# Kernel optimization log

Measured on AMD Instinct MI355X. Metric: run time of the kernel, lower is better.

## Reference

```python
import math
import jax, jax.numpy as jnp
import numpy as np

B, N, E, H = 1, 4096, 256, 8
D = E // H  # head dim = 32


def setup_inputs() -> dict:
    key = jax.random.key(0)
    ks = jax.random.split(key, 10)
    s = 1.0 / math.sqrt(E)
    return {
        "x": jax.random.normal(ks[0], (B, N, E), dtype=jnp.float32),
        "adjacency": jax.random.randint(ks[1], (B, N, N), 0, 2, dtype=jnp.int32),
        "Wq": jax.random.normal(ks[2], (E, E), dtype=jnp.float32) * s,
        "bq": jnp.zeros((E,), dtype=jnp.float32),
        "Wk": jax.random.normal(ks[3], (E, E), dtype=jnp.float32) * s,
        "bk": jnp.zeros((E,), dtype=jnp.float32),
        "Wv": jax.random.normal(ks[4], (E, E), dtype=jnp.float32) * s,
        "bv": jnp.zeros((E,), dtype=jnp.float32),
        "Wo": jax.random.normal(ks[5], (E, E), dtype=jnp.float32) * s,
        "bo": jnp.zeros((E,), dtype=jnp.float32),
    }


def reference(x, adjacency, Wq, bq, Wk, bk, Wv, bv, Wo, bo):
    b, n, e = x.shape
    # projections (torch Linear: x @ W.T + b), split into heads -> [B,H,N,D]
    def heads(y):
        return y.reshape(b, n, H, D).transpose(0, 2, 1, 3)
    q = heads(x @ Wq.T + bq)
    k = heads(x @ Wk.T + bk)
    v = heads(x @ Wv.T + bv)
    scores = jnp.einsum("bhnd,bhmd->bhnm", q, k) / math.sqrt(D)
    mask = (adjacency[:, None, :, :] == 0)  # [B,1,N,N]
    scores = jnp.where(mask, -jnp.inf, scores)
    w = jax.nn.softmax(scores, axis=-1)
    out = jnp.einsum("bhnm,bhmd->bhnd", w, v)
    out = out.transpose(0, 2, 1, 3).reshape(b, n, e)
    return out @ Wo.T + bo
```

## Files before the change

kernel.cpp:

```cpp
#include <hip/hip_runtime.h>
#include <math.h>


#define NTOK 4096
#define EDIM 256
#define HEADS 8
#define HD 32
#define NSPLIT 2
#define QSCALE 0.17677669529663687f
#define LOG2E 1.4426950408889634f
#define CINIT (-11.541560327111707f)

typedef __attribute__((ext_vector_type(8))) short bf16x8;
typedef __attribute__((ext_vector_type(4))) float f32x4;
typedef __attribute__((ext_vector_type(4))) unsigned long long u64x4;

typedef __attribute__((address_space(3))) unsigned char lds_u8;
typedef const __attribute__((address_space(1))) unsigned char gl_u8;

static __device__ inline short f2bf(float f) {
    unsigned u = __float_as_uint(f);
    u = (u + 0x7FFFu + ((u >> 16) & 1u)) >> 16;
    return (short)u;
}
static __device__ inline unsigned packtrunc(float a, float b) {
    return __builtin_amdgcn_perm(__float_as_uint(b), __float_as_uint(a),
                                 0x07060302u);
}
static __device__ inline float sel_mask(float v, unsigned long long m) {
    float r;
    asm("v_cndmask_b32 %0, 0, %1, %2" : "=v"(r) : "v"(v), "s"(m));
    return r;
}

__global__ __launch_bounds__(256) void prep(
    const int* __restrict__ adj, unsigned long long* __restrict__ maskT,
    const float* __restrict__ x,  const float* __restrict__ Wq,
    const float* __restrict__ Wk, const float* __restrict__ Wv,
    const float* __restrict__ Wo,
    short* __restrict__ xb,  short* __restrict__ wqb,
    short* __restrict__ wkb, short* __restrict__ wvb,
    short* __restrict__ wob)
{
    const int bid = blockIdx.x;
    if (bid < 2048) {
        const int wb = bid * 4 + (threadIdx.x >> 6);
        const int l = threadIdx.x & 63;
        const int lrow = l & 15;
        const int lc4 = ((l >> 4) & 3) * 4;
#pragma unroll
        for (int i = 0; i < 8; ++i) {
            const int w = wb + i * 8192;
            const int qb = w >> 8;
            const int kt = (w >> 2) & 63;
            const int b = w & 3;
            const int row = qb * 16 + lrow;
            const int col = kt * 64 + b * 16 + lc4;
            const int4 av = *(const int4*)&adj[row * NTOK + col];
            const unsigned long long m0 = __ballot(av.x != 0);
            const unsigned long long m1 = __ballot(av.y != 0);
            const unsigned long long m2 = __ballot(av.z != 0);
            const unsigned long long m3 = __ballot(av.w != 0);
            if (l == 0) {
                unsigned long long* dst = &maskT[(size_t)w * 4];
                dst[0] = m0; dst[1] = m1; dst[2] = m2; dst[3] = m3;
            }
        }
    } else {
        const int gid = (bid - 2048) * 256 + threadIdx.x;
        const int e = gid * 4;
        const float* src; short* dst; int off;
        if (e < NTOK * EDIM) { src = x; dst = xb; off = e; }
        else {
            const int r = e - NTOK * EDIM;
            const int wsel = r >> 16;
            off = r & 65535;
            src = (wsel == 0) ? Wq : (wsel == 1) ? Wk : (wsel == 2) ? Wv : Wo;
            dst = (wsel == 0) ? wqb : (wsel == 1) ? wkb : (wsel == 2) ? wvb : wob;
        }
        float4 v = *(const float4*)&src[off];
        uint2 t;
        t.x = (unsigned short)f2bf(v.x) | ((unsigned)(unsigned short)f2bf(v.y) << 16);
        t.y = (unsigned short)f2bf(v.z) | ((unsigned)(unsigned short)f2bf(v.w) << 16);
        *(uint2*)&dst[off] = t;
    }
}

__global__ __launch_bounds__(256) void qkv_mfma(
    const short* __restrict__ xb,
    const short* __restrict__ Wqb, const short* __restrict__ Wkb,
    const short* __restrict__ Wvb,
    const float* __restrict__ bq, const float* __restrict__ bk,
    const float* __restrict__ bv,
    short* __restrict__ qo, short* __restrict__ ko, short* __restrict__ vto)
{
    const int tid = threadIdx.x;
    const int wv = tid >> 6, lane = tid & 63;
    const int grp = lane >> 4, lcol = lane & 15;
    const int wsel = blockIdx.y >> 2;
    const int n0 = (blockIdx.y & 3) << 6;
    const int m0 = blockIdx.x * 64 + wv * 16;
    const short* __restrict__ W = (wsel == 0) ? Wqb : (wsel == 1) ? Wkb : Wvb;
    const float* __restrict__ bias = (wsel == 0) ? bq : (wsel == 1) ? bk : bv;

    bf16x8 af[8];
#pragma unroll
    for (int k = 0; k < 8; ++k)
        af[k] = *(const bf16x8*)&xb[(m0 + lcol) * 256 + k * 32 + grp * 8];

    f32x4 acc[4] = {};
#pragma unroll
    for (int k = 0; k < 8; ++k) {
#pragma unroll
        for (int t = 0; t < 4; ++t) {
            const bf16x8 bt =
                *(const bf16x8*)&W[(n0 + t * 16 + lcol) * 256 + k * 32 + grp * 8];
            acc[t] = __builtin_amdgcn_mfma_f32_16x16x32_bf16(af[k], bt, acc[t], 0, 0, 0);
        }
    }
#pragma unroll
    for (int t = 0; t < 4; ++t) {
        const int feat = n0 + t * 16 + lcol;
        const float bval = bias[feat];
        const int h = feat >> 5, d = feat & 31;
        if (wsel == 2) {
            uint2 o;
            o.x = (unsigned short)f2bf(acc[t][0] + bval) |
                  ((unsigned)(unsigned short)f2bf(acc[t][1] + bval) << 16);
            o.y = (unsigned short)f2bf(acc[t][2] + bval) |
                  ((unsigned)(unsigned short)f2bf(acc[t][3] + bval) << 16);
            *(uint2*)&vto[h * (HD * NTOK) + d * NTOK + m0 + grp * 4] = o;
        } else {
            short* __restrict__ out = (wsel == 0) ? qo : ko;
            const float sc = (wsel == 0) ? (QSCALE * LOG2E) : 1.0f;
#pragma unroll
            for (int j = 0; j < 4; ++j)
                out[h * (NTOK * HD) + (m0 + grp * 4 + j) * HD + d] =
                    f2bf((acc[t][j] + bval) * sc);
        }
    }
}

__global__ __launch_bounds__(256) void attn_mfma(
    const short* __restrict__ qg, const short* __restrict__ kg,
    const short* __restrict__ vtg, const unsigned long long* __restrict__ maskT,
    float* __restrict__ o_part, float* __restrict__ l_part)
{
    const int h = blockIdx.y;
    const int split = blockIdx.z;
    const int q0 = blockIdx.x << 6;
    const short* __restrict__ Q  = qg  + h * (NTOK * HD);
    const short* __restrict__ K  = kg  + h * (NTOK * HD);
    const short* __restrict__ Vt = vtg + h * (HD * NTOK);

    __shared__ short Ks[3][64][32];
    __shared__ short Vs[3][32][64];
    __shared__ short P_lds[4][16][76];

    const int tid = threadIdx.x;
    const int wv = tid >> 6;
    const int lane = tid & 63;
    const int grp = lane >> 4;
    const int lcol = lane & 15;
    const int q0w = q0 + wv * 16;
    const int wvu = __builtin_amdgcn_readfirstlane(wv);

    const int k_row = tid >> 2, k_oct = tid & 3;
    const int v_row = tid >> 3;
    const int v_oct = (tid & 7) ^ (v_row & 7);
    const short* __restrict__ kbase = &K[k_row * HD + k_oct * 8];
    const short* __restrict__ vbase = &Vt[v_row * NTOK + v_oct * 8];

    const bf16x8 qfrag = *(const bf16x8*)&Q[(q0w + lcol) * HD + grp * 8];

    const int qb = __builtin_amdgcn_readfirstlane(blockIdx.x * 4 + wv);
    const unsigned long long* __restrict__ mbase = maskT + (size_t)qb * 1024;

    f32x4 ot[2] = {};
    f32x4 lacc = {};
    const f32x4 cinit = {CINIT, CINIT, CINIT, CINIT};
    bf16x8 ones;
#pragma unroll
    for (int i = 0; i < 8; ++i) ones[i] = (short)0x3F80;

    const int tps = 64 / (int)gridDim.z;
    const int kt_begin = split * tps;
    const int kt_end = kt_begin + tps;

#define STAGE(BUF, KT)                                                       \
    {                                                                        \
        const int k0s = (KT) << 6;                                           \
        __builtin_amdgcn_global_load_lds(                                    \
            (gl_u8*)(kbase + k0s * HD),                                      \
            (lds_u8*)((unsigned char*)&Ks[BUF][0][0] + (wvu << 10)),         \
            16, 0, 0);                                                       \
        __builtin_amdgcn_global_load_lds(                                    \
            (gl_u8*)(vbase + k0s),                                           \
            (lds_u8*)((unsigned char*)&Vs[BUF][0][0] + (wvu << 10)),         \
            16, 0, 0);                                                       \
    }

    STAGE(0, kt_begin)
    if (kt_begin + 1 < kt_end) STAGE(1, kt_begin + 1)

    int cur = 0;
    for (int kt = kt_begin; kt < kt_end; ++kt) {
        if (kt + 1 < kt_end)
            asm volatile("s_waitcnt vmcnt(2)" ::: "memory");
        else
            asm volatile("s_waitcnt vmcnt(0)" ::: "memory");
        __builtin_amdgcn_s_barrier();
        __builtin_amdgcn_sched_barrier(0);

        const u64x4* mp = (const u64x4*)(mbase + kt * 16);
        const u64x4 wa = mp[0], wb = mp[1], wc = mp[2], wd = mp[3];

        const int nxt = (cur == 0) ? 2 : cur - 1;
        if (kt + 2 < kt_end) STAGE(nxt, kt + 2)

        bf16x8 kf[4], vf[4];
#pragma unroll
        for (int b = 0; b < 4; ++b)
            kf[b] = *(const bf16x8*)&Ks[cur][b * 16 + lcol][grp * 8];
#pragma unroll
        for (int c = 0; c < 2; ++c) {
            vf[c * 2 + 0] =
                *(const bf16x8*)&Vs[cur][c * 16 + lcol][(grp ^ (lcol & 7)) * 8];
            vf[c * 2 + 1] =
                *(const bf16x8*)&Vs[cur][c * 16 + lcol][((4 + grp) ^ (lcol & 7)) * 8];
        }

        f32x4 s[4];
        __builtin_amdgcn_s_setprio(1);
#pragma unroll
        for (int b = 0; b < 4; ++b)
            s[b] = __builtin_amdgcn_mfma_f32_16x16x32_bf16(
                kf[b], qfrag, cinit, 0, 0, 0);
        __builtin_amdgcn_s_setprio(0);

#pragma unroll
        for (int b = 0; b < 4; ++b) {
            const u64x4 wj = (b == 0) ? wa : (b == 1) ? wb : (b == 2) ? wc : wd;
            const float p0 = sel_mask(__builtin_amdgcn_exp2f(s[b][0]), wj[0]);
            const float p1 = sel_mask(__builtin_amdgcn_exp2f(s[b][1]), wj[1]);
            const float p2 = sel_mask(__builtin_amdgcn_exp2f(s[b][2]), wj[2]);
            const float p3 = sel_mask(__builtin_amdgcn_exp2f(s[b][3]), wj[3]);
            uint2 t;
            t.x = packtrunc(p0, p1);
            t.y = packtrunc(p2, p3);
            *(uint2*)&P_lds[wv][lcol][b * 16 + grp * 4] = t;
        }

        const uint2 pl0 = *(const uint2*)&P_lds[wv][lcol][grp * 8];
        const uint2 pl1 = *(const uint2*)&P_lds[wv][lcol][grp * 8 + 4];
        const uint2 pl2 = *(const uint2*)&P_lds[wv][lcol][32 + grp * 8];
        const uint2 pl3 = *(const uint2*)&P_lds[wv][lcol][32 + grp * 8 + 4];
        struct { uint2 a, b; } u0 = {pl0, pl1}, u1 = {pl2, pl3};
        const bf16x8 pf0 = __builtin_bit_cast(bf16x8, u0);
        const bf16x8 pf1 = __builtin_bit_cast(bf16x8, u1);

        __builtin_amdgcn_s_setprio(1);
#pragma unroll
        for (int c = 0; c < 2; ++c) {
            ot[c] = __builtin_amdgcn_mfma_f32_16x16x32_bf16(vf[c * 2 + 0], pf0, ot[c], 0, 0, 0);
            ot[c] = __builtin_amdgcn_mfma_f32_16x16x32_bf16(vf[c * 2 + 1], pf1, ot[c], 0, 0, 0);
        }
        lacc = __builtin_amdgcn_mfma_f32_16x16x32_bf16(ones, pf0, lacc, 0, 0, 0);
        lacc = __builtin_amdgcn_mfma_f32_16x16x32_bf16(ones, pf1, lacc, 0, 0, 0);
        __builtin_amdgcn_s_setprio(0);

        cur = (cur == 2) ? 0 : cur + 1;
    }
#undef STAGE

    float* __restrict__ ob = o_part + split * (NTOK * EDIM);
#pragma unroll
    for (int c = 0; c < 2; ++c) {
        float4 st;
        st.x = ot[c][0]; st.y = ot[c][1]; st.z = ot[c][2]; st.w = ot[c][3];
        *(float4*)&ob[(q0w + lcol) * EDIM + h * HD + c * 16 + grp * 4] = st;
    }
    if (grp == 0)
        l_part[split * (NTOK * HEADS) + (q0w + lcol) * HEADS + h] = lacc[0];
}

template <int NS>
__global__ __launch_bounds__(256) void out_mfma(
    const float* __restrict__ o_part, const float* __restrict__ l_part,
    const short* __restrict__ Wob, const float* __restrict__ bo,
    float* __restrict__ Y)
{
    const int tid = threadIdx.x;
    const int wv = tid >> 6, lane = tid & 63;
    const int grp = lane >> 4, lcol = lane & 15;
    const int n0 = blockIdx.y << 6;
    const int m0 = blockIdx.x * 64 + wv * 16;
    const int r = m0 + lcol;

    bf16x8 af[8];
#pragma unroll
    for (int k = 0; k < 8; ++k) {
        float4 s0 = {0.f, 0.f, 0.f, 0.f}, s1 = {0.f, 0.f, 0.f, 0.f};
        float lv = 0.f;
#pragma unroll
        for (int s = 0; s < NS; ++s) {
            const float* op = &o_part[s * (NTOK * EDIM) + r * EDIM + k * 32 + grp * 8];
            const float4 t0 = *(const float4*)op;
            const float4 t1 = *(const float4*)(op + 4);
            s0.x += t0.x; s0.y += t0.y; s0.z += t0.z; s0.w += t0.w;
            s1.x += t1.x; s1.y += t1.y; s1.z += t1.z; s1.w += t1.w;
            lv += l_part[s * (NTOK * HEADS) + r * HEADS + k];
        }
        const float inv = 1.0f / lv;
        bf16x8 t;
        t[0] = f2bf(s0.x * inv); t[1] = f2bf(s0.y * inv);
        t[2] = f2bf(s0.z * inv); t[3] = f2bf(s0.w * inv);
        t[4] = f2bf(s1.x * inv); t[5] = f2bf(s1.y * inv);
        t[6] = f2bf(s1.z * inv); t[7] = f2bf(s1.w * inv);
        af[k] = t;
    }

    f32x4 acc[4] = {};
#pragma unroll
    for (int k = 0; k < 8; ++k) {
#pragma unroll
        for (int t = 0; t < 4; ++t) {
            const bf16x8 bt =
                *(const bf16x8*)&Wob[(n0 + t * 16 + lcol) * 256 + k * 32 + grp * 8];
            acc[t] = __builtin_amdgcn_mfma_f32_16x16x32_bf16(af[k], bt, acc[t], 0, 0, 0);
        }
    }
#pragma unroll
    for (int t = 0; t < 4; ++t) {
        const float bval = bo[n0 + t * 16 + lcol];
#pragma unroll
        for (int j = 0; j < 4; ++j)
            Y[(m0 + grp * 4 + j) * EDIM + n0 + t * 16 + lcol] = acc[t][j] + bval;
    }
}

extern "C" void kernel_launch(void* const* d_in, const int* in_sizes, int n_in,
                              void* d_out, int out_size, void* d_ws, size_t ws_size,
                              hipStream_t stream) {
    (void)in_sizes; (void)n_in; (void)out_size; (void)ws_size;
    const float* x  = (const float*)d_in[0];
    const int*  adj = (const int*)d_in[1];
    const float* Wq = (const float*)d_in[2];
    const float* bq = (const float*)d_in[3];
    const float* Wk = (const float*)d_in[4];
    const float* bk = (const float*)d_in[5];
    const float* Wv = (const float*)d_in[6];
    const float* bv = (const float*)d_in[7];
    const float* Wo = (const float*)d_in[8];
    const float* bo = (const float*)d_in[9];

    char* ws = (char*)d_ws;
    short* x_bf  = (short*)(ws);
    short* q_ws  = (short*)(ws + (2u << 20));
    short* k_ws  = (short*)(ws + (4u << 20));
    short* vt_ws = (short*)(ws + (6u << 20));
    unsigned long long* maskT =
        (unsigned long long*)(ws + (8u << 20));
    short* Wq_bf = (short*)(ws + (10u << 20));
    short* Wk_bf = Wq_bf + (EDIM * EDIM);
    short* Wv_bf = Wk_bf + (EDIM * EDIM);
    short* Wo_bf = Wv_bf + (EDIM * EDIM);
    float* l_part = (float*)(ws + (11u << 20));
    float* o_part = (float*)(ws + (12u << 20));

    prep<<<dim3(2048 + 1280), 256, 0, stream>>>(
        adj, maskT, x, Wq, Wk, Wv, Wo, x_bf, Wq_bf, Wk_bf, Wv_bf, Wo_bf);
    qkv_mfma<<<dim3(64, 12), 256, 0, stream>>>(x_bf, Wq_bf, Wk_bf, Wv_bf,
                                               bq, bk, bv, q_ws, k_ws, vt_ws);
    attn_mfma<<<dim3(64, HEADS, NSPLIT), 256, 0, stream>>>(
        q_ws, k_ws, vt_ws, maskT, o_part, l_part);
    out_mfma<NSPLIT><<<dim3(64, 4), 256, 0, stream>>>(o_part, l_part, Wo_bf, bo,
                                                      (float*)d_out);
}
```

Before: 175.4 us.

## Process two KV tiles per barrier with a four-buffer pipeline

The attention main loop now handles two 64-key tiles per iteration, using four K/V LDS buffers and double-buffered P scratch. This halves the number of workgroup barriers and waitcnt points and lets two tiles' prefetch be issued together. In exchange it waits with vmcnt(0) every pair, which can expose load latency, and it raises LDS use, which may lower occupancy. It also assumes an even tile count per split.

```diff
diff --git a/kernel.cpp b/kernel.cpp
--- a/kernel.cpp
+++ b/kernel.cpp
@@ -153,9 +153,9 @@
     const short* __restrict__ K  = kg  + h * (NTOK * HD);
     const short* __restrict__ Vt = vtg + h * (HD * NTOK);
 
-    __shared__ short Ks[3][64][32];
-    __shared__ short Vs[3][32][64];
-    __shared__ short P_lds[4][16][76];
+    __shared__ short Ks[4][64][32];
+    __shared__ short Vs[4][32][64];
+    __shared__ short P_lds[2][4][16][76];
 
     const int tid = threadIdx.x;
     const int wv = tid >> 6;
@@ -200,78 +200,82 @@
             16, 0, 0);                                                       \
     }
 
+#define TILE(BUF, MP, PP)                                                    \
+    {                                                                        \
+        const u64x4 wa = (MP)[0], wb = (MP)[1], wc = (MP)[2], wd = (MP)[3];  \
+        bf16x8 kf[4], vf[4];                                                 \
+        _Pragma("unroll")                                                    \
+        for (int b = 0; b < 4; ++b)                                          \
+            kf[b] = *(const bf16x8*)&Ks[BUF][b * 16 + lcol][grp * 8];        \
+        _Pragma("unroll")                                                    \
+        for (int c = 0; c < 2; ++c) {                                        \
+            vf[c * 2 + 0] = *(const bf16x8*)                                 \
+                &Vs[BUF][c * 16 + lcol][(grp ^ (lcol & 7)) * 8];             \
+            vf[c * 2 + 1] = *(const bf16x8*)                                 \
+                &Vs[BUF][c * 16 + lcol][((4 + grp) ^ (lcol & 7)) * 8];       \
+        }                                                                    \
+        f32x4 s[4];                                                          \
+        __builtin_amdgcn_s_setprio(1);                                       \
+        _Pragma("unroll")                                                    \
+        for (int b = 0; b < 4; ++b)                                          \
+            s[b] = __builtin_amdgcn_mfma_f32_16x16x32_bf16(                  \
+                kf[b], qfrag, cinit, 0, 0, 0);                               \
+        __builtin_amdgcn_s_setprio(0);                                       \
+        _Pragma("unroll")                                                    \
+        for (int b = 0; b < 4; ++b) {                                        \
+            const u64x4 wj = (b == 0) ? wa : (b == 1) ? wb                   \
+                             : (b == 2) ? wc : wd;                           \
+            const float p0 = sel_mask(__builtin_amdgcn_exp2f(s[b][0]), wj[0]); \
+            const float p1 = sel_mask(__builtin_amdgcn_exp2f(s[b][1]), wj[1]); \
+            const float p2 = sel_mask(__builtin_amdgcn_exp2f(s[b][2]), wj[2]); \
+            const float p3 = sel_mask(__builtin_amdgcn_exp2f(s[b][3]), wj[3]); \
+            uint2 t;                                                         \
+            t.x = packtrunc(p0, p1);                                         \
+            t.y = packtrunc(p2, p3);                                         \
+            *(uint2*)&P_lds[PP][wv][lcol][b * 16 + grp * 4] = t;             \
+        }                                                                    \
+        const uint2 pl0 = *(const uint2*)&P_lds[PP][wv][lcol][grp * 8];      \
+        const uint2 pl1 = *(const uint2*)&P_lds[PP][wv][lcol][grp * 8 + 4];  \
+        const uint2 pl2 = *(const uint2*)&P_lds[PP][wv][lcol][32 + grp * 8]; \
+        const uint2 pl3 =                                                    \
+            *(const uint2*)&P_lds[PP][wv][lcol][32 + grp * 8 + 4];           \
+        struct { uint2 a, b; } u0 = {pl0, pl1}, u1 = {pl2, pl3};             \
+        const bf16x8 pf0 = __builtin_bit_cast(bf16x8, u0);                   \
+        const bf16x8 pf1 = __builtin_bit_cast(bf16x8, u1);                   \
+        __builtin_amdgcn_s_setprio(1);                                       \
+        _Pragma("unroll")                                                    \
+        for (int c = 0; c < 2; ++c) {                                        \
+            ot[c] = __builtin_amdgcn_mfma_f32_16x16x32_bf16(                 \
+                vf[c * 2 + 0], pf0, ot[c], 0, 0, 0);                         \
+            ot[c] = __builtin_amdgcn_mfma_f32_16x16x32_bf16(                 \
+                vf[c * 2 + 1], pf1, ot[c], 0, 0, 0);                         \
+        }                                                                    \
+        lacc = __builtin_amdgcn_mfma_f32_16x16x32_bf16(ones, pf0, lacc, 0, 0, 0); \
+        lacc = __builtin_amdgcn_mfma_f32_16x16x32_bf16(ones, pf1, lacc, 0, 0, 0); \
+        __builtin_amdgcn_s_setprio(0);                                       \
+    }
+
     STAGE(0, kt_begin)
-    if (kt_begin + 1 < kt_end) STAGE(1, kt_begin + 1)
-
-    int cur = 0;
-    for (int kt = kt_begin; kt < kt_end; ++kt) {
-        if (kt + 1 < kt_end)
-            asm volatile("s_waitcnt vmcnt(2)" ::: "memory");
-        else
-            asm volatile("s_waitcnt vmcnt(0)" ::: "memory");
+    STAGE(1, kt_begin + 1)
+
+    for (int kt = kt_begin; kt < kt_end; kt += 2) {
+        asm volatile("s_waitcnt vmcnt(0)" ::: "memory");
         __builtin_amdgcn_s_barrier();
         __builtin_amdgcn_sched_barrier(0);
 
-        const u64x4* mp = (const u64x4*)(mbase + kt * 16);
-        const u64x4 wa = mp[0], wb = mp[1], wc = mp[2], wd = mp[3];
-
-        const int nxt = (cur == 0) ? 2 : cur - 1;
-        if (kt + 2 < kt_end) STAGE(nxt, kt + 2)
-
-        bf16x8 kf[4], vf[4];
-#pragma unroll
-        for (int b = 0; b < 4; ++b)
-            kf[b] = *(const bf16x8*)&Ks[cur][b * 16 + lcol][grp * 8];
-#pragma unroll
-        for (int c = 0; c < 2; ++c) {
-            vf[c * 2 + 0] =
-                *(const bf16x8*)&Vs[cur][c * 16 + lcol][(grp ^ (lcol & 7)) * 8];
-            vf[c * 2 + 1] =
-                *(const bf16x8*)&Vs[cur][c * 16 + lcol][((4 + grp) ^ (lcol & 7)) * 8];
-        }
-
-        f32x4 s[4];
-        __builtin_amdgcn_s_setprio(1);
-#pragma unroll
-        for (int b = 0; b < 4; ++b)
-            s[b] = __builtin_amdgcn_mfma_f32_16x16x32_bf16(
-                kf[b], qfrag, cinit, 0, 0, 0);
-        __builtin_amdgcn_s_setprio(0);
-
-#pragma unroll
-        for (int b = 0; b < 4; ++b) {
-            const u64x4 wj = (b == 0) ? wa : (b == 1) ? wb : (b == 2) ? wc : wd;
-            const float p0 = sel_mask(__builtin_amdgcn_exp2f(s[b][0]), wj[0]);
-            const float p1 = sel_mask(__builtin_amdgcn_exp2f(s[b][1]), wj[1]);
-            const float p2 = sel_mask(__builtin_amdgcn_exp2f(s[b][2]), wj[2]);
-            const float p3 = sel_mask(__builtin_amdgcn_exp2f(s[b][3]), wj[3]);
-            uint2 t;
-            t.x = packtrunc(p0, p1);
-            t.y = packtrunc(p2, p3);
-            *(uint2*)&P_lds[wv][lcol][b * 16 + grp * 4] = t;
-        }
-
-        const uint2 pl0 = *(const uint2*)&P_lds[wv][lcol][grp * 8];
-        const uint2 pl1 = *(const uint2*)&P_lds[wv][lcol][grp * 8 + 4];
-        const uint2 pl2 = *(const uint2*)&P_lds[wv][lcol][32 + grp * 8];
-        const uint2 pl3 = *(const uint2*)&P_lds[wv][lcol][32 + grp * 8 + 4];
-        struct { uint2 a, b; } u0 = {pl0, pl1}, u1 = {pl2, pl3};
-        const bf16x8 pf0 = __builtin_bit_cast(bf16x8, u0);
-        const bf16x8 pf1 = __builtin_bit_cast(bf16x8, u1);
-
-        __builtin_amdgcn_s_setprio(1);
-#pragma unroll
-        for (int c = 0; c < 2; ++c) {
-            ot[c] = __builtin_amdgcn_mfma_f32_16x16x32_bf16(vf[c * 2 + 0], pf0, ot[c], 0, 0, 0);
-            ot[c] = __builtin_amdgcn_mfma_f32_16x16x32_bf16(vf[c * 2 + 1], pf1, ot[c], 0, 0, 0);
-        }
-        lacc = __builtin_amdgcn_mfma_f32_16x16x32_bf16(ones, pf0, lacc, 0, 0, 0);
-        lacc = __builtin_amdgcn_mfma_f32_16x16x32_bf16(ones, pf1, lacc, 0, 0, 0);
-        __builtin_amdgcn_s_setprio(0);
-
-        cur = (cur == 2) ? 0 : cur + 1;
+        const u64x4* mpA = (const u64x4*)(mbase + kt * 16);
+        const u64x4* mpB = (const u64x4*)(mbase + kt * 16 + 16);
+
+        if (kt + 2 < kt_end) {
+            STAGE((kt + 2) & 3, kt + 2)
+            STAGE((kt + 3) & 3, kt + 3)
+        }
+
+        TILE(kt & 3, mpA, 0)
+        TILE((kt + 1) & 3, mpB, 1)
     }
 #undef STAGE
+#undef TILE
 
     float* __restrict__ ob = o_part + split * (NTOK * EDIM);
 #pragma unroll
```

After: 187.4 us. 6.8% more time.
